# Kernel optimization log

Measured on AMD Instinct MI355X. Metric: run time of the kernel, lower is better.

Reference implementation:

```python
import jax, jax.numpy as jnp
import numpy as np

B, V, D, P = 32, 21, 512, 64
IN, OUT = D * P, 720
E, K, R, H = 8, 2, 16, 256
SCALING = 16.0 / R  # lora alpha / rank = 1.0
TEMP = 1.0


def setup_inputs() -> dict:
    key = jax.random.key(0)
    ks = jax.random.split(key, 9)
    s = lambda k, shape, fan: jax.random.normal(k, shape, dtype=jnp.float32) * (1.0 / np.sqrt(fan))
    return {
        "x": jax.random.normal(ks[0], (B, V, D, P), dtype=jnp.float32),
        "W_base": s(ks[1], (OUT, IN), IN),
        "b_base": s(ks[2], (OUT,), IN),
        "W_r1": s(ks[3], (H, D), D),
        "b_r1": s(ks[4], (H,), D),
        "W_r2": s(ks[5], (E, H), H),
        "b_r2": s(ks[6], (E,), H),
        "lora_A": s(ks[7], (E, R, IN), IN),
        "lora_B": s(ks[8], (E, OUT, R), R),
    }


def reference(x, W_base, b_base, W_r1, b_r1, W_r2, b_r2, lora_A, lora_B):
    # base head: flatten last two dims -> linear (dropout is identity in eval)
    flattened = x.reshape(B, V, IN)                      # [B, V, D*P]
    base_out = flattened @ W_base.T + b_base             # [B, V, OUT]

    # learned router on pooled features (dropout identity, no noise in eval)
    pooled = x.mean(axis=(1, 3))                         # [B, D]
    h = jax.nn.gelu(pooled @ W_r1.T + b_r1, approximate=False)
    logits = h @ W_r2.T + b_r2                           # [B, E]
    probs = jax.nn.softmax(logits / TEMP, axis=-1)
    topk_w, topk_idx = jax.lax.top_k(probs, K)           # [B, K]
    topk_w = topk_w / jnp.clip(topk_w.sum(-1, keepdims=True), 1e-6)

    # all LoRA experts on all samples (matches original), then gather top-k
    flat2d = flattened.reshape(B * V, IN)
    low = jnp.einsum('ni,eri->enr', flat2d, lora_A)      # [E, BV, R]
    delta = jnp.einsum('enr,eor->eno', low, lora_B) * SCALING  # [E, BV, OUT]
    stack = delta.reshape(E, B, V, OUT).transpose(1, 0, 2, 3)  # [B, E, V, OUT]
    sel = jnp.take_along_axis(stack, topk_idx[:, :, None, None], axis=1)  # [B, K, V, OUT]
    moe_delta = (topk_w[:, :, None, None] * sel).sum(axis=1)  # [B, V, OUT]

    return base_out + moe_delta, probs
```

## Files before the change

kernel.cpp:

```cpp
#include <hip/hip_runtime.h>
#include <math.h>

constexpr int Bz = 32, Vz = 21, Dz = 512, Pz = 64;
constexpr int INz = Dz * Pz;
constexpr int OUTz = 720;
constexpr int Ez = 8, Rz = 16, Hz = 256;
constexpr int Mz = Bz * Vz;
constexpr int Nz = OUTz + Ez * Rz;
constexpr int Kz = INz;

constexpr int BM = 128, BN = 128, BK = 32;
constexpr int SPLIT = 32;
constexpr int KSL = Kz / SPLIT;
constexpr int NCH = KSL / BK;
constexpr int LDA = 40;

typedef _Float16 f16x8 __attribute__((ext_vector_type(8)));
typedef __fp16  fp16x2 __attribute__((ext_vector_type(2)));
typedef float f32x4 __attribute__((ext_vector_type(4)));

__device__ __forceinline__ unsigned int cvt2(float a, float b) {
    fp16x2 p = __builtin_amdgcn_cvt_pkrtz(a, b);
    return __builtin_bit_cast(unsigned int, p);
}

__device__ __forceinline__ void barrier_lgkm() {
    asm volatile("s_waitcnt lgkmcnt(0)\n\ts_barrier" ::: "memory");
}

__global__ __launch_bounds__(256, 3)
void gemm_pool_kernel(const float* __restrict__ x, const float* __restrict__ Wb,
                      const float* __restrict__ lA, float* __restrict__ C,
                      float* __restrict__ pooled)
{
    __shared__ _Float16 As[2][BM * LDA];
    __shared__ _Float16 Bs[2][BN * LDA];
    __shared__ float plocal[BM][16];

    const int id = blockIdx.x;
    const int x8 = id & 7;
    const int k8 = id >> 3;
    const int nt = k8 % 7;
    const int mt = (k8 / 7) % 6;
    const int s  = (k8 / 42) * 8 + x8;

    const int t  = threadIdx.x;
    const int r  = t >> 1;
    const int h  = t & 1;
    const int kbase = s * KSL + h * 16;

    int gm = mt * BM + r;
    const bool mval = (gm < Mz);
    if (!mval) gm = Mz - 1;
    const float* pa = x + (size_t)gm * Kz + kbase;

    int gn = nt * BN + r;
    if (gn >= Nz) gn = Nz - 1;
    const float* pb = (gn < OUTz) ? (Wb + (size_t)gn * Kz + kbase)
                                  : (lA + (size_t)(gn - OUTz) * Kz + kbase);

    const int wave = t >> 6, lane = t & 63;
    const int wr = (wave >> 1) * 64;
    const int wc = (wave & 1) * 64;
    const int fl = lane & 15;
    const int ko = (lane >> 4) * 8;

    f32x4 acc[4][4] = {};

    float4 ca[2][4], cb[2][4];
    #pragma unroll
    for (int q = 0; q < 4; ++q) {
        ca[0][q] = *(const float4*)(pa + 4 * q);
        cb[0][q] = *(const float4*)(pb + 4 * q);
        ca[1][q] = *(const float4*)(pa + BK + 4 * q);
        cb[1][q] = *(const float4*)(pb + BK + 4 * q);
    }

    const bool do_pool = (nt == 0) && mval;
    float psum = 0.0f;

#define GSTEP(SET, CIDX)                                                          \
    {                                                                             \
        const int c_ = (CIDX);                                                    \
        if (do_pool) {                                                            \
            psum += (ca[SET][0].x + ca[SET][0].y + ca[SET][0].z + ca[SET][0].w)   \
                  + (ca[SET][1].x + ca[SET][1].y + ca[SET][1].z + ca[SET][1].w)   \
                  + (ca[SET][2].x + ca[SET][2].y + ca[SET][2].z + ca[SET][2].w)   \
                  + (ca[SET][3].x + ca[SET][3].y + ca[SET][3].z + ca[SET][3].w);  \
        }                                                                         \
        if (SET == 1) {                                                           \
            float ps2 = psum + __shfl_down(psum, 1, 64);                          \
            if (do_pool && h == 0) plocal[r][c_ >> 1] = ps2;                      \
            psum = 0.0f;                                                          \
        }                                                                         \
        _Float16* wA = &As[SET][r * LDA + h * 16];                                \
        *((uint4*)wA)     = make_uint4(                                           \
            cvt2(ca[SET][0].x, ca[SET][0].y), cvt2(ca[SET][0].z, ca[SET][0].w),   \
            cvt2(ca[SET][1].x, ca[SET][1].y), cvt2(ca[SET][1].z, ca[SET][1].w));  \
        *((uint4*)wA + 1) = make_uint4(                                           \
            cvt2(ca[SET][2].x, ca[SET][2].y), cvt2(ca[SET][2].z, ca[SET][2].w),   \
            cvt2(ca[SET][3].x, ca[SET][3].y), cvt2(ca[SET][3].z, ca[SET][3].w));  \
        _Float16* wB = &Bs[SET][r * LDA + h * 16];                                \
        *((uint4*)wB)     = make_uint4(                                           \
            cvt2(cb[SET][0].x, cb[SET][0].y), cvt2(cb[SET][0].z, cb[SET][0].w),   \
            cvt2(cb[SET][1].x, cb[SET][1].y), cvt2(cb[SET][1].z, cb[SET][1].w));  \
        *((uint4*)wB + 1) = make_uint4(                                           \
            cvt2(cb[SET][2].x, cb[SET][2].y), cvt2(cb[SET][2].z, cb[SET][2].w),   \
            cvt2(cb[SET][3].x, cb[SET][3].y), cvt2(cb[SET][3].z, cb[SET][3].w));  \
        if (c_ + 2 < NCH) {           \
            const float* qa = pa + (c_ + 2) * BK;                                 \
            const float* qb = pb + (c_ + 2) * BK;                                 \
            _Pragma("unroll")                                                     \
            for (int q = 0; q < 4; ++q) {                                         \
                ca[SET][q] = *(const float4*)(qa + 4 * q);                        \
                cb[SET][q] = *(const float4*)(qb + 4 * q);                        \
            }                                                                     \
        }                                                                         \
        barrier_lgkm();                                                           \
        f16x8 af[4], bfr[4];                                                      \
        _Pragma("unroll")                                                         \
        for (int i = 0; i < 4; ++i)                                               \
            af[i] = *(const f16x8*)(&As[SET][(wr + i * 16 + fl) * LDA + ko]);     \
        _Pragma("unroll")                                                         \
        for (int j = 0; j < 4; ++j)                                               \
            bfr[j] = *(const f16x8*)(&Bs[SET][(wc + j * 16 + fl) * LDA + ko]);    \
        _Pragma("unroll")                                                         \
        for (int i = 0; i < 4; ++i)                                               \
            _Pragma("unroll")                                                     \
            for (int j = 0; j < 4; ++j)                                           \
                acc[i][j] = __builtin_amdgcn_mfma_f32_16x16x32_f16(               \
                                af[i], bfr[j], acc[i][j], 0, 0, 0);               \
    }

    for (int cc = 0; cc < NCH; cc += 2) {
        GSTEP(0, cc)
        GSTEP(1, cc + 1)
    }
#undef GSTEP

    if (nt == 0) {
        __syncthreads();
        for (int idx = t; idx < BM * 16; idx += 256) {
            const int rr = idx >> 4, j = idx & 15;
            const int g = mt * BM + rr;
            if (g < Mz) atomicAdd(&pooled[(g / Vz) * Dz + s * 16 + j], plocal[rr][j]);
        }
    }

    const int rq = (lane >> 4) * 4;
    #pragma unroll
    for (int i = 0; i < 4; ++i) {
        const int gmr0 = mt * BM + wr + i * 16 + rq;
        #pragma unroll
        for (int j = 0; j < 4; ++j) {
            const int gnc = nt * BN + wc + j * 16 + fl;
            if (gnc < Nz) {
                #pragma unroll
                for (int q2 = 0; q2 < 4; ++q2) {
                    const int gmr = gmr0 + q2;
                    if (gmr < Mz) atomicAdd(&C[(size_t)gmr * Nz + gnc], acc[i][j][q2]);
                }
            }
        }
    }
}

__global__ __launch_bounds__(256)
void router_kernel(const float* __restrict__ pooled_raw,
                   const float* __restrict__ Wr1, const float* __restrict__ br1,
                   const float* __restrict__ Wr2, const float* __restrict__ br2,
                   float* __restrict__ probs_out, int* __restrict__ tki, float* __restrict__ tkw)
{
    const int b = blockIdx.x, t = threadIdx.x;
    const int wave = t >> 6, lane = t & 63;
    __shared__ float hbuf[Hz];
    __shared__ float lg[Ez];

    const float sc = 1.0f / (float)(Vz * Pz);
    float pv[8];
    const float* prow = pooled_raw + b * Dz + lane * 8;
    #pragma unroll
    for (int u = 0; u < 8; ++u) pv[u] = prow[u] * sc;

    for (int i0 = 0; i0 < 64; i0 += 4) {
        float v[4];
        #pragma unroll
        for (int u = 0; u < 4; ++u) {
            const int j = wave * 64 + i0 + u;
            const float* wrow = Wr1 + (size_t)j * Dz + lane * 8;
            float4 w0 = *(const float4*)(wrow);
            float4 w1 = *(const float4*)(wrow + 4);
            v[u] = pv[0]*w0.x + pv[1]*w0.y + pv[2]*w0.z + pv[3]*w0.w
                 + pv[4]*w1.x + pv[5]*w1.y + pv[6]*w1.z + pv[7]*w1.w;
        }
        #pragma unroll
        for (int u = 0; u < 4; ++u) {
            #pragma unroll
            for (int off = 32; off >= 1; off >>= 1) v[u] += __shfl_down(v[u], off, 64);
        }
        if (lane == 0) {
            #pragma unroll
            for (int u = 0; u < 4; ++u) {
                const int j = wave * 64 + i0 + u;
                float a = v[u] + br1[j];
                hbuf[j] = 0.5f * a * (1.0f + erff(a * 0.70710678118654752440f));
            }
        }
    }
    __syncthreads();

    if (t < Ez) {
        const float* w = Wr2 + (size_t)t * Hz;
        float a = br2[t];
        for (int j = 0; j < Hz; ++j) a = fmaf(hbuf[j], w[j], a);
        lg[t] = a;
    }
    __syncthreads();

    if (t == 0) {
        float mx = lg[0];
        for (int e = 1; e < Ez; ++e) mx = fmaxf(mx, lg[e]);
        float p[Ez], ssum = 0.0f;
        for (int e = 0; e < Ez; ++e) { p[e] = expf(lg[e] - mx); ssum += p[e]; }
        const float inv = 1.0f / ssum;
        for (int e = 0; e < Ez; ++e) { p[e] *= inv; probs_out[b * Ez + e] = p[e]; }
        int i0 = 0;
        for (int e = 1; e < Ez; ++e) if (p[e] > p[i0]) i0 = e;
        int i1 = (i0 == 0) ? 1 : 0;
        for (int e = 0; e < Ez; ++e) if (e != i0 && p[e] > p[i1]) i1 = e;
        float s2 = p[i0] + p[i1];
        if (s2 < 1e-6f) s2 = 1e-6f;
        tki[b * 2] = i0; tki[b * 2 + 1] = i1;
        tkw[b * 2] = p[i0] / s2; tkw[b * 2 + 1] = p[i1] / s2;
    }
}

__global__ __launch_bounds__(256)
void combine_kernel(const float* __restrict__ C, const float* __restrict__ bb,
                    const float* __restrict__ loraB,
                    const int* __restrict__ tki, const float* __restrict__ tkw,
                    float* __restrict__ out)
{
    const int m = blockIdx.x;
    const int t = threadIdx.x;
    const int b = m / Vz;
    const int e0 = tki[b * 2], e1 = tki[b * 2 + 1];
    const float w0 = tkw[b * 2], w1 = tkw[b * 2 + 1];

    __shared__ float lw[2 * Rz];
    if (t < 2 * Rz) {
        const int e = (t < Rz) ? e0 : e1;
        lw[t] = C[(size_t)m * Nz + OUTz + e * Rz + (t & (Rz - 1))];
    }
    __syncthreads();

    for (int o = t; o < OUTz; o += 256) {
        float acc = C[(size_t)m * Nz + o] + bb[o];
        const float* B0 = loraB + ((size_t)e0 * OUTz + o) * Rz;
        const float* B1 = loraB + ((size_t)e1 * OUTz + o) * Rz;
        float d0 = 0.0f, d1 = 0.0f;
        #pragma unroll
        for (int rr = 0; rr < Rz; ++rr) {
            d0 = fmaf(lw[rr], B0[rr], d0);
            d1 = fmaf(lw[Rz + rr], B1[rr], d1);
        }
        out[(size_t)m * OUTz + o] = acc + w0 * d0 + w1 * d1;
    }
}

extern "C" void kernel_launch(void* const* d_in, const int* in_sizes, int n_in,
                              void* d_out, int out_size, void* d_ws, size_t ws_size,
                              hipStream_t stream)
{
    const float* x   = (const float*)d_in[0];
    const float* Wb  = (const float*)d_in[1];
    const float* bb  = (const float*)d_in[2];
    const float* Wr1 = (const float*)d_in[3];
    const float* br1 = (const float*)d_in[4];
    const float* Wr2 = (const float*)d_in[5];
    const float* br2 = (const float*)d_in[6];
    const float* lA  = (const float*)d_in[7];
    const float* lB  = (const float*)d_in[8];
    float* out = (float*)d_out;

    float* C      = (float*)d_ws;
    float* pooled = C + (size_t)Mz * Nz;
    int*   tki    = (int*)(pooled + Bz * Dz);
    float* tkw    = (float*)(tki + 2 * Bz);

    (void)hipMemsetAsync(d_ws, 0, ((size_t)Mz * Nz + Bz * Dz) * sizeof(float), stream);

    gemm_pool_kernel<<<dim3(7 * 6 * SPLIT), 256, 0, stream>>>(x, Wb, lA, C, pooled);
    router_kernel<<<Bz, 256, 0, stream>>>(pooled, Wr1, br1, Wr2, br2,
                                          out + (size_t)Mz * OUTz, tki, tkw);
    combine_kernel<<<Mz, 256, 0, stream>>>(C, bb, lB, tki, tkw, out);
}
```

Baseline: 377.0 us.

## Replace split-K atomic accumulation with per-split partial buffers reduced in combine

Halves the split-K factor and, when the workspace is large enough, writes each split's GEMM tile to its own partial buffer with plain stores instead of global atomics. The combine kernel then sums the partials, so the full-output memset and the atomic contention go away. The LDS row pad also shrinks from 40 to 36 halves. The cost is extra workspace traffic, since the combine reads SPLIT copies of C, and fewer blocks give less parallelism; the old atomic path remains as a fallback.

```diff
diff --git a/kernel.cpp b/kernel.cpp
--- a/kernel.cpp
+++ b/kernel.cpp
@@ -10,10 +10,10 @@
 constexpr int Kz = INz;
 
 constexpr int BM = 128, BN = 128, BK = 32;
-constexpr int SPLIT = 32;
+constexpr int SPLIT = 16;
 constexpr int KSL = Kz / SPLIT;
 constexpr int NCH = KSL / BK;
-constexpr int LDA = 40;
+constexpr int LDA = 36;
 
 typedef _Float16 f16x8 __attribute__((ext_vector_type(8)));
 typedef __fp16  fp16x2 __attribute__((ext_vector_type(2)));
@@ -28,14 +28,15 @@
     asm volatile("s_waitcnt lgkmcnt(0)\n\ts_barrier" ::: "memory");
 }
 
+template <bool PART>
 __global__ __launch_bounds__(256, 3)
 void gemm_pool_kernel(const float* __restrict__ x, const float* __restrict__ Wb,
-                      const float* __restrict__ lA, float* __restrict__ C,
-                      float* __restrict__ pooled)
+                      const float* __restrict__ lA, float* __restrict__ part,
+                      float* __restrict__ C, float* __restrict__ pooled)
 {
     __shared__ _Float16 As[2][BM * LDA];
     __shared__ _Float16 Bs[2][BN * LDA];
-    __shared__ float plocal[BM][16];
+    __shared__ float plocal[BM][NCH / 2];
 
     const int id = blockIdx.x;
     const int x8 = id & 7;
@@ -88,7 +89,7 @@
                   + (ca[SET][2].x + ca[SET][2].y + ca[SET][2].z + ca[SET][2].w)   \
                   + (ca[SET][3].x + ca[SET][3].y + ca[SET][3].z + ca[SET][3].w);  \
         }                                                                         \
-        if (SET == 1) {                                                           \
+        if (SET == 1) {           \
             float ps2 = psum + __shfl_down(psum, 1, 64);                          \
             if (do_pool && h == 0) plocal[r][c_ >> 1] = ps2;                      \
             psum = 0.0f;                                                          \
@@ -107,7 +108,7 @@
         *((uint4*)wB + 1) = make_uint4(                                           \
             cvt2(cb[SET][2].x, cb[SET][2].y), cvt2(cb[SET][2].z, cb[SET][2].w),   \
             cvt2(cb[SET][3].x, cb[SET][3].y), cvt2(cb[SET][3].z, cb[SET][3].w));  \
-        if (c_ + 2 < NCH) {           \
+        if (c_ + 2 < NCH) {                                                       \
             const float* qa = pa + (c_ + 2) * BK;                                 \
             const float* qb = pb + (c_ + 2) * BK;                                 \
             _Pragma("unroll")                                                     \
@@ -140,14 +141,15 @@
 
     if (nt == 0) {
         __syncthreads();
-        for (int idx = t; idx < BM * 16; idx += 256) {
-            const int rr = idx >> 4, j = idx & 15;
+        for (int idx = t; idx < BM * (NCH / 2); idx += 256) {
+            const int rr = idx / (NCH / 2), j = idx % (NCH / 2);
             const int g = mt * BM + rr;
-            if (g < Mz) atomicAdd(&pooled[(g / Vz) * Dz + s * 16 + j], plocal[rr][j]);
+            if (g < Mz) atomicAdd(&pooled[(g / Vz) * Dz + s * (NCH / 2) + j], plocal[rr][j]);
         }
     }
 
     const int rq = (lane >> 4) * 4;
+    float* dst = PART ? (part + (size_t)s * Mz * Nz) : C;
     #pragma unroll
     for (int i = 0; i < 4; ++i) {
         const int gmr0 = mt * BM + wr + i * 16 + rq;
@@ -158,7 +160,10 @@
                 #pragma unroll
                 for (int q2 = 0; q2 < 4; ++q2) {
                     const int gmr = gmr0 + q2;
-                    if (gmr < Mz) atomicAdd(&C[(size_t)gmr * Nz + gnc], acc[i][j][q2]);
+                    if (gmr < Mz) {
+                        if (PART) dst[(size_t)gmr * Nz + gnc] = acc[i][j][q2];
+                        else      atomicAdd(&dst[(size_t)gmr * Nz + gnc], acc[i][j][q2]);
+                    }
                 }
             }
         }
@@ -235,9 +240,10 @@
     }
 }
 
+template <bool PART>
 __global__ __launch_bounds__(256)
-void combine_kernel(const float* __restrict__ C, const float* __restrict__ bb,
-                    const float* __restrict__ loraB,
+void combine_kernel(const float* __restrict__ part, const float* __restrict__ C,
+                    const float* __restrict__ bb, const float* __restrict__ loraB,
                     const int* __restrict__ tki, const float* __restrict__ tkw,
                     float* __restrict__ out)
 {
@@ -250,12 +256,23 @@
     __shared__ float lw[2 * Rz];
     if (t < 2 * Rz) {
         const int e = (t < Rz) ? e0 : e1;
-        lw[t] = C[(size_t)m * Nz + OUTz + e * Rz + (t & (Rz - 1))];
+        const size_t off = (size_t)m * Nz + OUTz + e * Rz + (t & (Rz - 1));
+        float v = 0.0f;
+        if (PART) {
+            #pragma unroll
+            for (int ss = 0; ss < SPLIT; ++ss) v += part[(size_t)ss * Mz * Nz + off];
+        } else v = C[off];
+        lw[t] = v;
     }
     __syncthreads();
 
     for (int o = t; o < OUTz; o += 256) {
-        float acc = C[(size_t)m * Nz + o] + bb[o];
+        float acc = bb[o];
+        if (PART) {
+            #pragma unroll
+            for (int ss = 0; ss < SPLIT; ++ss)
+                acc += part[(size_t)ss * Mz * Nz + (size_t)m * Nz + o];
+        } else acc += C[(size_t)m * Nz + o];
         const float* B0 = loraB + ((size_t)e0 * OUTz + o) * Rz;
         const float* B1 = loraB + ((size_t)e1 * OUTz + o) * Rz;
         float d0 = 0.0f, d1 = 0.0f;
@@ -283,15 +300,35 @@
     const float* lB  = (const float*)d_in[8];
     float* out = (float*)d_out;
 
-    float* C      = (float*)d_ws;
-    float* pooled = C + (size_t)Mz * Nz;
-    int*   tki    = (int*)(pooled + Bz * Dz);
-    float* tkw    = (float*)(tki + 2 * Bz);
-
-    (void)hipMemsetAsync(d_ws, 0, ((size_t)Mz * Nz + Bz * Dz) * sizeof(float), stream);
-
-    gemm_pool_kernel<<<dim3(7 * 6 * SPLIT), 256, 0, stream>>>(x, Wb, lA, C, pooled);
-    router_kernel<<<Bz, 256, 0, stream>>>(pooled, Wr1, br1, Wr2, br2,
-                                          out + (size_t)Mz * OUTz, tki, tkw);
-    combine_kernel<<<Mz, 256, 0, stream>>>(C, bb, lB, tki, tkw, out);
-}
+    const size_t part_elems = (size_t)SPLIT * Mz * Nz;
+    const size_t need = (part_elems + Bz * Dz + 256) * sizeof(float);
+    const bool use_part = (ws_size >= need);
+
+    if (use_part) {
+        float* part   = (float*)d_ws;
+        float* pooled = part + part_elems;
+        int*   tki    = (int*)(pooled + Bz * Dz);
+        float* tkw    = (float*)(tki + 2 * Bz);
+
+        (void)hipMemsetAsync(pooled, 0, Bz * Dz * sizeof(float), stream);
+
+        gemm_pool_kernel<true><<<dim3(7 * 6 * SPLIT), 256, 0, stream>>>(
+            x, Wb, lA, part, nullptr, pooled);
+        router_kernel<<<Bz, 256, 0, stream>>>(pooled, Wr1, br1, Wr2, br2,
+                                              out + (size_t)Mz * OUTz, tki, tkw);
+        combine_kernel<true><<<Mz, 256, 0, stream>>>(part, nullptr, bb, lB, tki, tkw, out);
+    } else {
+        float* C      = (float*)d_ws;
+        float* pooled = C + (size_t)Mz * Nz;
+        int*   tki    = (int*)(pooled + Bz * Dz);
+        float* tkw    = (float*)(tki + 2 * Bz);
+
+        (void)hipMemsetAsync(d_ws, 0, ((size_t)Mz * Nz + Bz * Dz) * sizeof(float), stream);
+
+        gemm_pool_kernel<false><<<dim3(7 * 6 * SPLIT), 256, 0, stream>>>(
+            x, Wb, lA, nullptr, C, pooled);
+        router_kernel<<<Bz, 256, 0, stream>>>(pooled, Wr1, br1, Wr2, br2,
+                                              out + (size_t)Mz * OUTz, tki, tkw);
+        combine_kernel<false><<<Mz, 256, 0, stream>>>(nullptr, C, bb, lB, tki, tkw, out);
+    }
+}
```

Result: faster. 362.8 us (-3.8%).
